# Optimization experiments

Hardware: AMD Instinct MI355X
Metric: run time of the kernel (lower is better)

## Reference

```python
import jax, jax.numpy as jnp
import numpy as np

NEG_SLOPE = 0.01  # torch leaky_relu default

def _lrelu(x):
    return jax.nn.leaky_relu(x, NEG_SLOPE)

def _l2norm(x, axis):
    # torch F.normalize(p=2, eps=1e-12)
    n = jnp.linalg.norm(x, axis=axis, keepdims=True)
    return x / jnp.maximum(n, 1e-12)

def setup_inputs() -> dict:
    key = jax.random.key(0)
    ks = jax.random.split(key, 12)
    Nda, Nq, C, Din, Dout = 10000, 64, 1024, 128, 256
    target_adj = (jax.random.uniform(ks[0], (Nda, Nda)) < 0.002).astype(jnp.float32)
    query_adj = (jax.random.uniform(ks[1], (Nq, Nq)) < 0.2).astype(jnp.float32)
    node_features_da = jax.random.normal(ks[2], (Nda, Din), dtype=jnp.float32)
    node_features_q = jax.random.normal(ks[3], (Nq, Din), dtype=jnp.float32)
    candidate_set = jax.random.randint(ks[4], (C,), 0, Nda)
    candidate_adj = (jax.random.uniform(ks[5], (C, C)) < 0.01).astype(jnp.float32)
    s_in = 1.0 / np.sqrt(Din).astype(np.float32)
    s_out = 1.0 / np.sqrt(Dout).astype(np.float32)
    W1_da = jax.random.normal(ks[6], (Din, Dout), dtype=jnp.float32) * s_in
    W1_q = jax.random.normal(ks[7], (Din, Dout), dtype=jnp.float32) * s_in
    W2_da = jax.random.normal(ks[8], (Dout, Dout), dtype=jnp.float32) * s_out
    W2_q = jax.random.normal(ks[9], (Dout, Dout), dtype=jnp.float32) * s_out
    threshold = jnp.float32(0.2)
    return {"target_adj": target_adj, "node_features_da": node_features_da,
            "query_adj": query_adj, "node_features_q": node_features_q,
            "candidate_set": candidate_set, "candidate_adj": candidate_adj,
            "threshold": threshold, "W1_da": W1_da, "W1_q": W1_q,
            "W2_da": W2_da, "W2_q": W2_q}

def _cross_cosine(q, da, candidate_set):
    # cosine similarity between each query node and each candidate target node: [Nq, C]
    return _l2norm(q, 1) @ _l2norm(da[candidate_set], 1).T

def reference(target_adj, node_features_da, query_adj, node_features_q,
              candidate_set, candidate_adj, threshold, W1_da, W1_q, W2_da, W2_q):
    # layer 1: GCN propagation on both graphs (gcn(adj,x) = adj @ x @ W)
    da1 = _lrelu(target_adj @ (node_features_da @ W1_da))   # [Nda, D]
    q1 = _lrelu(query_adj @ (node_features_q @ W1_q))       # [Nq, D]
    c1 = _cross_cosine(q1, da1, candidate_set)               # [Nq, C]
    pre_da1 = da1[candidate_set]                             # [C, D]
    # NOTE: da1[candidate_set].data = ... mutates a temporary in torch -> no-op on da1
    att_da1 = _lrelu(da1)                                    # dropout in eval = identity
    h1_q = c1 @ pre_da1                                      # [Nq, D]
    att_q1 = _lrelu(q1 + _l2norm(h1_q, 0))
    # layer 2
    da2 = _lrelu(target_adj @ (att_da1 @ W2_da))
    q2 = _lrelu(query_adj @ (att_q1 @ W2_q))
    c2 = _cross_cosine(q2, da2, candidate_set)
    pre_da2 = da2[candidate_set]
    att_da2 = _lrelu(da2)                                    # in-place update is again a no-op
    h2_q = c2 @ pre_da2
    att_q2 = _lrelu(q2 + _l2norm(h2_q, 0))
    # graph-level matching score per target node
    emb = jnp.mean(att_q2, axis=0, keepdims=True)            # [1, D]
    num = att_da2 @ emb[0]                                   # [Nda]
    den = jnp.maximum(jnp.linalg.norm(att_da2, axis=1) * jnp.linalg.norm(emb), 1e-8)
    end = (num / den)[None, :]                               # [1, Nda]
    # threshold selection expressed with a mask (jit-safe, same math: excluded
    # rows/cols are zero and do not affect L2 norms, sums, or the trace)
    m = (end[0] > threshold).astype(att_da2.dtype)           # [Nda]
    F_ = att_da2 * m[:, None]
    re_adj = F_ @ F_.T                                       # [Nda, Nda]
    nor_re = _l2norm(re_adj, 1) * target_adj                 # elementwise with original adj
    cnt = jnp.sum(m)
    total = jnp.sum(nor_re)
    tr = jnp.trace(nor_re)
    has = cnt > 0
    pre_avg_degree = jnp.where(has, total / jnp.maximum(cnt, 1.0), 0.0)
    pre_avg_nodes = jnp.where(has, tr, 0.0)
    pre_density = jnp.where(has, 2.0 * total / (tr * (tr - 1.0) + 1e-4), 0.0)
    return (end, att_da2, att_q2, pre_avg_degree, pre_density, pre_avg_nodes)
```

## Files before the change

kernel.cpp:

```cpp
#include <hip/hip_runtime.h>

constexpr int NDA = 10000;
constexpr int NQ  = 64;
constexpr int CND = 1024;
constexpr int DIN = 128;
constexpr int D   = 256;
constexpr int CAP = 96;
constexpr int NT128 = (NDA + 127) / 128;
constexpr int NB128 = NT128 * 2;
constexpr int NCHUNK = 32;
constexpr int GCHUNK = 320;

#define LRELU(x) ((x) >= 0.f ? (x) : 0.01f * (x))

__device__ __forceinline__ float wave_red64(float v) {
#pragma unroll
    for (int o = 32; o; o >>= 1) v += __shfl_down(v, o);
    return v;
}

struct GemmSmem    { float As[32][65]; float Bs[32][68]; };
struct Gemm128Smem { float As[16][132]; float Bs[16][132]; };
struct CrossSmem   { float qs[D]; float cmw[256]; int sci[256]; float red[4]; float sqn; };
struct SpmmSmem    { int sc[CAP]; };
struct CsrSmem     { int scnt; };
struct EndSmem     { float se[D]; float scnt; float red[4]; };
struct FinalSmem   { int sc[CAP]; float smask[CAP]; int sdiag; float r1[4], r2[4], r3[4]; };
struct Attq4Smem   { float hbuf[64][65]; float red[4][64]; float invs[64]; };
union SMem {
    GemmSmem g; Gemm128Smem h; CrossSmem c; SpmmSmem s; CsrSmem z;
    EndSmem e; FinalSmem f; Attq4Smem a;
};

template <bool RELU_A, bool RELU_C>
__device__ __forceinline__ void gemm_body(GemmSmem& sm, int bx, int by,
                                          const float* __restrict__ A,
                                          const float* __restrict__ B,
                                          float* __restrict__ C,
                                          int M, int N, int K) {
    const int bm = bx * 64, bn = by * 64;
    const int tid = threadIdx.x;
    const int tx = tid & 15, ty = tid >> 4;
    const int lm = tid >> 2, lk = (tid & 3) * 8;
    const int kb = tid >> 3, nb = (tid & 7) * 8;
    const bool aValid = (bm + lm) < M;
    const float* aPtr = A + (size_t)(bm + lm) * K + lk;
    const float* bPtr = B + (size_t)kb * N + bn + nb;
    float4 ra0 = make_float4(0.f, 0.f, 0.f, 0.f), ra1 = ra0, rb0, rb1;
    if (aValid) { ra0 = *(const float4*)aPtr; ra1 = *(const float4*)(aPtr + 4); }
    rb0 = *(const float4*)bPtr;
    rb1 = *(const float4*)(bPtr + 4);
    float acc[4][4] = {};
    for (int k0 = 0; k0 < K; k0 += 32) {
        float4 wa0 = ra0, wa1 = ra1, wb0 = rb0, wb1 = rb1;
        if (RELU_A) {
            wa0.x = LRELU(wa0.x); wa0.y = LRELU(wa0.y); wa0.z = LRELU(wa0.z); wa0.w = LRELU(wa0.w);
            wa1.x = LRELU(wa1.x); wa1.y = LRELU(wa1.y); wa1.z = LRELU(wa1.z); wa1.w = LRELU(wa1.w);
        }
        sm.As[lk + 0][lm] = wa0.x; sm.As[lk + 1][lm] = wa0.y;
        sm.As[lk + 2][lm] = wa0.z; sm.As[lk + 3][lm] = wa0.w;
        sm.As[lk + 4][lm] = wa1.x; sm.As[lk + 5][lm] = wa1.y;
        sm.As[lk + 6][lm] = wa1.z; sm.As[lk + 7][lm] = wa1.w;
        *(float4*)&sm.Bs[kb][nb]     = wb0;
        *(float4*)&sm.Bs[kb][nb + 4] = wb1;
        __syncthreads();
        if (k0 + 32 < K) {
            if (aValid) {
                ra0 = *(const float4*)(aPtr + k0 + 32);
                ra1 = *(const float4*)(aPtr + k0 + 36);
            }
            rb0 = *(const float4*)(bPtr + (size_t)(k0 + 32) * N);
            rb1 = *(const float4*)(bPtr + (size_t)(k0 + 32) * N + 4);
        }
#pragma unroll
        for (int kk = 0; kk < 32; kk++) {
            float av[4], bv[4];
#pragma unroll
            for (int i = 0; i < 4; i++) av[i] = sm.As[kk][ty * 4 + i];
#pragma unroll
            for (int j = 0; j < 4; j++) bv[j] = sm.Bs[kk][tx * 4 + j];
#pragma unroll
            for (int i = 0; i < 4; i++)
#pragma unroll
                for (int j = 0; j < 4; j++) acc[i][j] += av[i] * bv[j];
        }
        __syncthreads();
    }
#pragma unroll
    for (int i = 0; i < 4; i++) {
        int r = bm + ty * 4 + i;
        if (r < M) {
            float4 v = make_float4(acc[i][0], acc[i][1], acc[i][2], acc[i][3]);
            if (RELU_C) { v.x = LRELU(v.x); v.y = LRELU(v.y); v.z = LRELU(v.z); v.w = LRELU(v.w); }
            *(float4*)(C + (size_t)r * N + bn + tx * 4) = v;
        }
    }
}

template <bool RELU_A>
__device__ __forceinline__ void gemm128_body(Gemm128Smem& sm, int bx, int by,
                                             const float* __restrict__ A,
                                             const float* __restrict__ B,
                                             float* __restrict__ C,
                                             int M, int N, int K) {
    const int bm = bx * 128, bn = by * 128;
    const int tid = threadIdx.x;
    const int tx = tid & 15, ty = tid >> 4;
    const int am = tid >> 1, ak = (tid & 1) * 8;
    const int bk = tid >> 4, bn8 = (tid & 15) * 8;
    const bool aValid = (bm + am) < M;
    const float* aPtr = A + (size_t)(bm + am) * K + ak;
    const float* bPtr = B + (size_t)bk * N + bn + bn8;
    float4 ra0 = make_float4(0.f, 0.f, 0.f, 0.f), ra1 = ra0, rb0, rb1;
    if (aValid) { ra0 = *(const float4*)aPtr; ra1 = *(const float4*)(aPtr + 4); }
    rb0 = *(const float4*)bPtr;
    rb1 = *(const float4*)(bPtr + 4);
    float acc[8][8] = {};
    for (int k0 = 0; k0 < K; k0 += 16) {
        float a8[8] = { ra0.x, ra0.y, ra0.z, ra0.w, ra1.x, ra1.y, ra1.z, ra1.w };
        if (RELU_A) {
#pragma unroll
            for (int j = 0; j < 8; j++) a8[j] = LRELU(a8[j]);
        }
#pragma unroll
        for (int j = 0; j < 8; j++) sm.As[ak + j][am] = a8[j];
        *(float4*)&sm.Bs[bk][bn8]     = rb0;
        *(float4*)&sm.Bs[bk][bn8 + 4] = rb1;
        __syncthreads();
        if (k0 + 16 < K) {
            if (aValid) {
                ra0 = *(const float4*)(aPtr + k0 + 16);
                ra1 = *(const float4*)(aPtr + k0 + 20);
            }
            rb0 = *(const float4*)(bPtr + (size_t)(k0 + 16) * N);
            rb1 = *(const float4*)(bPtr + (size_t)(k0 + 16) * N + 4);
        }
#pragma unroll
        for (int kk = 0; kk < 16; kk++) {
            float4 a0 = *(const float4*)&sm.As[kk][ty * 8];
            float4 a1 = *(const float4*)&sm.As[kk][ty * 8 + 4];
            float4 b0 = *(const float4*)&sm.Bs[kk][tx * 8];
            float4 b1 = *(const float4*)&sm.Bs[kk][tx * 8 + 4];
            float av[8] = { a0.x, a0.y, a0.z, a0.w, a1.x, a1.y, a1.z, a1.w };
            float bv[8] = { b0.x, b0.y, b0.z, b0.w, b1.x, b1.y, b1.z, b1.w };
#pragma unroll
            for (int i = 0; i < 8; i++)
#pragma unroll
                for (int j = 0; j < 8; j++) acc[i][j] += av[i] * bv[j];
        }
        __syncthreads();
    }
#pragma unroll
    for (int i = 0; i < 8; i++) {
        int r = bm + ty * 8 + i;
        if (r < M) {
            float4 v0 = make_float4(acc[i][0], acc[i][1], acc[i][2], acc[i][3]);
            float4 v1 = make_float4(acc[i][4], acc[i][5], acc[i][6], acc[i][7]);
            *(float4*)(C + (size_t)r * N + bn + tx * 8)     = v0;
            *(float4*)(C + (size_t)r * N + bn + tx * 8 + 4) = v1;
        }
    }
}

__device__ __forceinline__ void csr_body(CsrSmem& sm, const float* __restrict__ adj,
                                         int* __restrict__ cols,
                                         int* __restrict__ rowcnt, int row) {
    if (threadIdx.x == 0) sm.scnt = 0;
    __syncthreads();
    const float4* rp = (const float4*)(adj + (size_t)row * NDA);
    for (int i = threadIdx.x; i < NDA / 4; i += 256) {
        float4 v = rp[i];
        if (v.x != 0.f) { int s = atomicAdd(&sm.scnt, 1); if (s < CAP) cols[row * CAP + s] = 4 * i; }
        if (v.y != 0.f) { int s = atomicAdd(&sm.scnt, 1); if (s < CAP) cols[row * CAP + s] = 4 * i + 1; }
        if (v.z != 0.f) { int s = atomicAdd(&sm.scnt, 1); if (s < CAP) cols[row * CAP + s] = 4 * i + 2; }
        if (v.w != 0.f) { int s = atomicAdd(&sm.scnt, 1); if (s < CAP) cols[row * CAP + s] = 4 * i + 3; }
    }
    __syncthreads();
    if (threadIdx.x == 0) rowcnt[row] = min(sm.scnt, CAP);
}

__device__ __forceinline__ void spmm_body(SpmmSmem& sm, const int* __restrict__ cols,
                                          const int* __restrict__ rowcnt,
                                          const float* __restrict__ X,
                                          float* __restrict__ out1,
                                          float* __restrict__ out2, int row) {
    int d = threadIdx.x;
    int cnt = rowcnt[row];
    if (d < cnt) sm.sc[d] = cols[row * CAP + d];
    __syncthreads();
    float a0 = 0.f, a1 = 0.f, a2 = 0.f, a3 = 0.f;
    int k = 0;
    for (; k + 4 <= cnt; k += 4) {
        a0 += X[(size_t)sm.sc[k + 0] * D + d];
        a1 += X[(size_t)sm.sc[k + 1] * D + d];
        a2 += X[(size_t)sm.sc[k + 2] * D + d];
        a3 += X[(size_t)sm.sc[k + 3] * D + d];
    }
    for (; k < cnt; k++) a0 += X[(size_t)sm.sc[k] * D + d];
    float v = LRELU(a0 + a1 + a2 + a3);
    out1[(size_t)row * D + d] = v;
    if (out2) out2[(size_t)row * D + d] = LRELU(v);
}

__device__ __forceinline__ void cross_body(CrossSmem& sm, const float* __restrict__ q,
                                           const float* __restrict__ da,
                                           const int* __restrict__ cand,
                                           float* __restrict__ hpart,
                                           int r, int qr) {
    int d = threadIdx.x;
    float qv = q[r * D + d];
    sm.qs[d] = qv;
    sm.sci[d] = cand[qr * 256 + d];
    float p = wave_red64(qv * qv);
    int w = d >> 6, lane = d & 63;
    if (lane == 0) sm.red[w] = p;
    __syncthreads();
    if (d == 0) sm.sqn = fmaxf(sqrtf(sm.red[0] + sm.red[1] + sm.red[2] + sm.red[3]), 1e-12f);
    __syncthreads();
    float qn = sm.sqn;
    {
        const float4* ap = (const float4*)(da + (size_t)sm.sci[d] * D);
        float dot = 0.f, sq = 0.f;
#pragma unroll 8
        for (int k = 0; k < D / 4; k++) {
            float4 v = ap[k];
            dot += sm.qs[4 * k] * v.x + sm.qs[4 * k + 1] * v.y + sm.qs[4 * k + 2] * v.z + sm.qs[4 * k + 3] * v.w;
            sq  += v.x * v.x + v.y * v.y + v.z * v.z + v.w * v.w;
        }
        sm.cmw[d] = dot / (qn * fmaxf(sqrtf(sq), 1e-12f));
    }
    __syncthreads();
    float a0 = 0.f, a1 = 0.f, a2 = 0.f, a3 = 0.f, a4 = 0.f, a5 = 0.f, a6 = 0.f, a7 = 0.f;
    for (int c = 0; c < 256; c += 8) {
        a0 += sm.cmw[c + 0] * da[(size_t)sm.sci[c + 0] * D + d];
        a1 += sm.cmw[c + 1] * da[(size_t)sm.sci[c + 1] * D + d];
        a2 += sm.cmw[c + 2] * da[(size_t)sm.sci[c + 2] * D + d];
        a3 += sm.cmw[c + 3] * da[(size_t)sm.sci[c + 3] * D + d];
        a4 += sm.cmw[c + 4] * da[(size_t)sm.sci[c + 4] * D + d];
        a5 += sm.cmw[c + 5] * da[(size_t)sm.sci[c + 5] * D + d];
        a6 += sm.cmw[c + 6] * da[(size_t)sm.sci[c + 6] * D + d];
        a7 += sm.cmw[c + 7] * da[(size_t)sm.sci[c + 7] * D + d];
    }
    hpart[((size_t)qr * NQ + r) * D + d] = ((a0 + a1) + (a2 + a3)) + ((a4 + a5) + (a6 + a7));
}

__global__ __launch_bounds__(256) void stage0_kernel(const float* __restrict__ adj,
                                                     int* __restrict__ cols,
                                                     int* __restrict__ rowcnt,
                                                     const float* __restrict__ Fda,
                                                     const float* __restrict__ W1da,
                                                     float* __restrict__ X1,
                                                     const float* __restrict__ Fq,
                                                     const float* __restrict__ W1q,
                                                     float* __restrict__ Xq) {
    __shared__ SMem sm;
    int bid = blockIdx.x;
    if (bid < NB128) {
        gemm128_body<false>(sm.h, bid >> 1, bid & 1, Fda, W1da, X1, NDA, D, DIN);
    } else if (bid < NB128 + 4) {
        gemm_body<false, false>(sm.g, 0, bid - NB128, Fq, W1q, Xq, NQ, D, DIN);
    } else {
        csr_body(sm.z, adj, cols, rowcnt, bid - (NB128 + 4));
    }
}

__global__ __launch_bounds__(256) void stage_sg_kernel(const int* __restrict__ cols,
                                                       const int* __restrict__ rowcnt,
                                                       const float* __restrict__ X,
                                                       float* __restrict__ out1,
                                                       float* __restrict__ out2,
                                                       const float* __restrict__ Aq,
                                                       const float* __restrict__ Bq,
                                                       float* __restrict__ Cq) {
    __shared__ SMem sm;
    int bid = blockIdx.x;
    if (bid < 4) {
        gemm_body<false, true>(sm.g, 0, bid, Aq, Bq, Cq, NQ, D, NQ);
    } else {
        spmm_body(sm.s, cols, rowcnt, X, out1, out2, bid - 4);
    }
}

__global__ __launch_bounds__(256) void mergeA_kernel(const float* __restrict__ q1,
                                                     const float* __restrict__ da1,
                                                     const int* __restrict__ cand,
                                                     float* __restrict__ hpart,
                                                     const float* __restrict__ W2da,
                                                     float* __restrict__ Y2) {
    __shared__ SMem sm;
    int bid = blockIdx.x;
    if (bid < 256) {
        cross_body(sm.c, q1, da1, cand, hpart, bid >> 2, bid & 3);
    } else {
        int t = bid - 256;
        gemm128_body<true>(sm.h, t >> 1, t & 1, da1, W2da, Y2, NDA, D, D);
    }
}

__global__ __launch_bounds__(256) void cross_kernel(const float* __restrict__ q,
                                                    const float* __restrict__ da,
                                                    const int* __restrict__ cand,
                                                    float* __restrict__ hpart) {
    __shared__ SMem sm;
    cross_body(sm.c, q, da, cand, hpart, blockIdx.x, blockIdx.y);
}

__global__ __launch_bounds__(256) void qfused_kernel(const float* __restrict__ q,
                                                     const float* __restrict__ hpart,
                                                     const float* __restrict__ W2q,
                                                     float* __restrict__ Zq) {
    __shared__ float aqT[D][65];
    __shared__ float Bs[32][68];
    int d = threadIdx.x;
    float hv[NQ];
    float ss = 0.f;
#pragma unroll
    for (int r = 0; r < NQ; r++) {
        float h = hpart[(size_t)r * D + d]
                + hpart[(size_t)(NQ + r) * D + d]
                + hpart[(size_t)(2 * NQ + r) * D + d]
                + hpart[(size_t)(3 * NQ + r) * D + d];
        hv[r] = h;
        ss += h * h;
    }
    float inv = 1.f / fmaxf(sqrtf(ss), 1e-12f);
#pragma unroll
    for (int r = 0; r < NQ; r++) {
        float v = q[r * D + d] + hv[r] * inv;
        aqT[d][r] = LRELU(v);
    }
    __syncthreads();
    const int bn = blockIdx.x * 64;
    const int tx = d & 15, ty = d >> 4;
    const int kb = d >> 3, nb = (d & 7) * 8;
    float acc[4][4] = {};
    for (int k0 = 0; k0 < D; k0 += 32) {
        float4 b0 = *(const float4*)(W2q + (size_t)(k0 + kb) * D + bn + nb);
        float4 b1 = *(const float4*)(W2q + (size_t)(k0 + kb) * D + bn + nb + 4);
        *(float4*)&Bs[kb][nb]     = b0;
        *(float4*)&Bs[kb][nb + 4] = b1;
        __syncthreads();
#pragma unroll
        for (int kk = 0; kk < 32; kk++) {
            float av[4], bv[4];
#pragma unroll
            for (int i = 0; i < 4; i++) av[i] = aqT[k0 + kk][ty * 4 + i];
#pragma unroll
            for (int j = 0; j < 4; j++) bv[j] = Bs[kk][tx * 4 + j];
#pragma unroll
            for (int i = 0; i < 4; i++)
#pragma unroll
                for (int j = 0; j < 4; j++) acc[i][j] += av[i] * bv[j];
        }
        __syncthreads();
    }
#pragma unroll
    for (int i = 0; i < 4; i++) {
        float4 v = make_float4(acc[i][0], acc[i][1], acc[i][2], acc[i][3]);
        *(float4*)(Zq + (size_t)(ty * 4 + i) * D + bn + tx * 4) = v;
    }
}

__global__ __launch_bounds__(256) void attq4_kernel(const float* __restrict__ q,
                                                    const float* __restrict__ hpart,
                                                    float* __restrict__ attq,
                                                    float* __restrict__ emb,
                                                    float* __restrict__ cnt,
                                                    double* __restrict__ tot,
                                                    double* __restrict__ tr,
                                                    int* __restrict__ done) {
    __shared__ SMem smu;
    Attq4Smem& sm = smu.a;
    int b = blockIdx.x, t = threadIdx.x;
    int lc = t & 63, rq = t >> 6;
    int c = b * 64 + lc;
    if (b == 0 && t == 0) { *cnt = 0.f; *tot = 0.0; *tr = 0.0; *done = 0; }
    float ss = 0.f;
#pragma unroll
    for (int rr = 0; rr < 16; rr++) {
        int r = rq * 16 + rr;
        float h = hpart[(size_t)r * D + c]
                + hpart[(size_t)(NQ + r) * D + c]
                + hpart[(size_t)(2 * NQ + r) * D + c]
                + hpart[(size_t)(3 * NQ + r) * D + c];
        sm.hbuf[r][lc] = h;
        ss += h * h;
    }
    sm.red[rq][lc] = ss;
    __syncthreads();
    if (rq == 0) {
        float s = sm.red[0][lc] + sm.red[1][lc] + sm.red[2][lc] + sm.red[3][lc];
        sm.invs[lc] = 1.f / fmaxf(sqrtf(s), 1e-12f);
    }
    __syncthreads();
    float inv = sm.invs[lc];
    float es = 0.f;
#pragma unroll
    for (int rr = 0; rr < 16; rr++) {
        int r = rq * 16 + rr;
        float v = q[r * D + c] + sm.hbuf[r][lc] * inv;
        v = LRELU(v);
        attq[r * D + c] = v;
        es += v;
    }
    __syncthreads();
    sm.red[rq][lc] = es;
    __syncthreads();
    if (rq == 0) {
        float e = (sm.red[0][lc] + sm.red[1][lc] + sm.red[2][lc] + sm.red[3][lc]) * (1.f / (float)NQ);
        emb[c] = e;
    }
}

__global__ __launch_bounds__(256) void end_kernel(const float* __restrict__ A,
                                                  const float* __restrict__ emb,
                                                  const float* __restrict__ thr_p,
                                                  float* __restrict__ endv,
                                                  float* __restrict__ m,
                                                  float* __restrict__ cnt) {
    __shared__ SMem smu;
    EndSmem& sm = smu.e;
    int d = threadIdx.x;
    float ev = emb[d];
    sm.se[d] = ev;
    if (d == 0) sm.scnt = 0.f;
    int w = d >> 6, lane = d & 63;
    float pe = wave_red64(ev * ev);
    if (lane == 0) sm.red[w] = pe;
    __syncthreads();
    float embn = sqrtf(sm.red[0] + sm.red[1] + sm.red[2] + sm.red[3]);
    float thr = *thr_p;
    int row = blockIdx.x * 4 + w;
    const float* ar = A + (size_t)row * D;
    float num = 0.f, sq = 0.f;
#pragma unroll
    for (int s = 0; s < 4; s++) {
        float v = ar[lane + 64 * s];
        num += v * sm.se[lane + 64 * s];
        sq += v * v;
    }
#pragma unroll
    for (int o = 32; o; o >>= 1) { num += __shfl_down(num, o); sq += __shfl_down(sq, o); }
    if (lane == 0) {
        float den = fmaxf(sqrtf(sq) * embn, 1e-8f);
        float e = num / den;
        endv[row] = e;
        float mv = e > thr ? 1.f : 0.f;
        m[row] = mv;
        if (mv != 0.f) atomicAdd(&sm.scnt, 1.f);
    }
    __syncthreads();
    if (d == 0 && sm.scnt != 0.f) atomicAdd(cnt, sm.scnt);
}

__global__ __launch_bounds__(256) void Gpart_kernel(const float* __restrict__ A,
                                                    const float* __restrict__ m,
                                                    float* __restrict__ Gp) {
    __shared__ SMem smu;
    Gemm128Smem& sm = smu.h;
    int ti = blockIdx.x >> 1, tj = blockIdx.x & 1;
    int base = blockIdx.y * GCHUNK;
    int tid = threadIdx.x;
    int tx = tid & 15, ty = tid >> 4;
    int sr = tid >> 4, sc8 = (tid & 15) * 8;
    float acc[8][8] = {};
    for (int g0 = 0; g0 < GCHUNK; g0 += 16) {
        int r = base + g0 + sr;
        float4 va0 = make_float4(0.f, 0.f, 0.f, 0.f), va1 = va0, vb0 = va0, vb1 = va0;
        float mv = 0.f;
        if (r < NDA) {
            mv = m[r];
            const float* ar = A + (size_t)r * D;
            va0 = *(const float4*)(ar + ti * 128 + sc8);
            va1 = *(const float4*)(ar + ti * 128 + sc8 + 4);
            vb0 = *(const float4*)(ar + tj * 128 + sc8);
            vb1 = *(const float4*)(ar + tj * 128 + sc8 + 4);
        }
        va0.x *= mv; va0.y *= mv; va0.z *= mv; va0.w *= mv;
        va1.x *= mv; va1.y *= mv; va1.z *= mv; va1.w *= mv;
        *(float4*)&sm.As[sr][sc8]     = va0;
        *(float4*)&sm.As[sr][sc8 + 4] = va1;
        *(float4*)&sm.Bs[sr][sc8]     = vb0;
        *(float4*)&sm.Bs[sr][sc8 + 4] = vb1;
        __syncthreads();
#pragma unroll
        for (int kk = 0; kk < 16; kk++) {
            float4 a0 = *(const float4*)&sm.As[kk][ty * 8];
            float4 a1 = *(const float4*)&sm.As[kk][ty * 8 + 4];
            float4 b0 = *(const float4*)&sm.Bs[kk][tx * 8];
            float4 b1 = *(const float4*)&sm.Bs[kk][tx * 8 + 4];
            float av[8] = { a0.x, a0.y, a0.z, a0.w, a1.x, a1.y, a1.z, a1.w };
            float bv[8] = { b0.x, b0.y, b0.z, b0.w, b1.x, b1.y, b1.z, b1.w };
#pragma unroll
            for (int i = 0; i < 8; i++)
#pragma unroll
                for (int j = 0; j < 8; j++) acc[i][j] += av[i] * bv[j];
        }
        __syncthreads();
    }
    float* gp = Gp + (size_t)blockIdx.y * D * D;
#pragma unroll
    for (int i = 0; i < 8; i++) {
        int gi = ti * 128 + ty * 8 + i;
        float4 v0 = make_float4(acc[i][0], acc[i][1], acc[i][2], acc[i][3]);
        float4 v1 = make_float4(acc[i][4], acc[i][5], acc[i][6], acc[i][7]);
        *(float4*)(gp + (size_t)gi * D + tj * 128 + tx * 8)     = v0;
        *(float4*)(gp + (size_t)gi * D + tj * 128 + tx * 8 + 4) = v1;
    }
}

__global__ __launch_bounds__(256) void Gred_kernel(const float* __restrict__ Gp,
                                                   float* __restrict__ G) {
    int idx = blockIdx.x * 256 + threadIdx.x;
    float s = 0.f;
#pragma unroll
    for (int c = 0; c < NCHUNK; c++) s += Gp[(size_t)c * D * D + idx];
    G[idx] = s;
}

__global__ __launch_bounds__(256) void gemmH_kernel(const float* __restrict__ A,
                                                    const float* __restrict__ B,
                                                    float* __restrict__ C) {
    __shared__ SMem sm;
    gemm128_body<false>(sm.h, blockIdx.x >> 1, blockIdx.x & 1, A, B, C, NDA, D, D);
}

__global__ __launch_bounds__(256) void final_kernel(const int* __restrict__ cols,
                                                    const int* __restrict__ rowcnt,
                                                    const float* __restrict__ m,
                                                    const float* __restrict__ A,
                                                    const float* __restrict__ H,
                                                    double* __restrict__ total,
                                                    double* __restrict__ tr,
                                                    float* __restrict__ cnt,
                                                    int* __restrict__ done,
                                                    float* __restrict__ o_sc) {
    __shared__ SMem smu;
    FinalSmem& sm = smu.f;
    int i = blockIdx.x;
    int d = threadIdx.x;
    if (m[i] != 0.f) {
        int cnt_r = rowcnt[i];
        if (d == 0) sm.sdiag = 0;
        if (d < cnt_r) {
            int j = cols[i * CAP + d];
            sm.sc[d] = j;
            sm.smask[d] = m[j];
            if (j == i) sm.sdiag = 1;
        }
        __syncthreads();
        float av = A[(size_t)i * D + d];
        float hv = H[(size_t)i * D + d];
        float sd = 0.f;
        for (int k = 0; k < cnt_r; k++)
            if (sm.smask[k] != 0.f) sd += A[(size_t)sm.sc[k] * D + d];
        float p1 = av * sd, p2 = av * hv, p3 = av * av;
#pragma unroll
        for (int o = 32; o; o >>= 1) {
            p1 += __shfl_down(p1, o);
            p2 += __shfl_down(p2, o);
            p3 += __shfl_down(p3, o);
        }
        int w = d >> 6, lane = d & 63;
        if (lane == 0) { sm.r1[w] = p1; sm.r2[w] = p2; sm.r3[w] = p3; }
        __syncthreads();
        if (d == 0) {
            float num  = sm.r1[0] + sm.r1[1] + sm.r1[2] + sm.r1[3];
            float den2 = sm.r2[0] + sm.r2[1] + sm.r2[2] + sm.r2[3];
            float self = sm.r3[0] + sm.r3[1] + sm.r3[2] + sm.r3[3];
            float denom = fmaxf(sqrtf(den2), 1e-12f);
            double inv = 1.0 / (double)denom;
            if (num != 0.f) atomicAdd(total, (double)num * inv);
            if (sm.sdiag) atomicAdd(tr, (double)self * inv);
        }
    }
    if (d == 0) {
        __threadfence();
        int prev = atomicAdd(done, 1);
        if (prev == NDA - 1) {
            float c = atomicAdd(cnt, 0.f);
            float T = (float)atomicAdd(total, 0.0);
            float R = (float)atomicAdd(tr, 0.0);
            bool has = c > 0.f;
            o_sc[0] = has ? (T / fmaxf(c, 1.f)) : 0.f;
            o_sc[1] = has ? (2.f * T / (R * (R - 1.f) + 1e-4f)) : 0.f;
            o_sc[2] = has ? R : 0.f;
        }
    }
}

extern "C" void kernel_launch(void* const* d_in, const int* in_sizes, int n_in,
                              void* d_out, int out_size, void* d_ws, size_t ws_size,
                              hipStream_t stream) {
    (void)in_sizes; (void)n_in; (void)out_size; (void)ws_size;
    const float* adj  = (const float*)d_in[0];
    const float* Fda  = (const float*)d_in[1];
    const float* Qadj = (const float*)d_in[2];
    const float* Fq   = (const float*)d_in[3];
    const int*   cand = (const int*)d_in[4];
    const float* thr  = (const float*)d_in[6];
    const float* W1da = (const float*)d_in[7];
    const float* W1q  = (const float*)d_in[8];
    const float* W2da = (const float*)d_in[9];
    const float* W2q  = (const float*)d_in[10];

    float* out = (float*)d_out;
    float* o_end    = out;
    float* o_attda2 = out + NDA;
    float* o_attq2  = out + NDA + (size_t)NDA * D;
    float* o_sc     = o_attq2 + NQ * D;

    char* w = (char*)d_ws;
    size_t off = 0;
    auto alloc = [&](size_t b) { size_t r = off; off += (b + 255) & ~(size_t)255; return r; };
    float* bufA = (float*)(w + alloc((size_t)NDA * D * 4));
    float* bufB = (float*)(w + alloc((size_t)NDA * D * 4));
    float* bufC = (float*)(w + alloc((size_t)NDA * D * 4));
    int* colsb   = (int*)(w + alloc((size_t)NDA * CAP * 4));
    int* rowcntb = (int*)(w + alloc((size_t)NDA * 4));
    float* mbuf  = (float*)(w + alloc((size_t)NDA * 4));
    float* Gb    = (float*)(w + alloc((size_t)D * D * 4));
    float* Gp    = (float*)(w + alloc((size_t)NCHUNK * D * D * 4));
    char* zbase = w + alloc(256);
    float* cntb  = (float*)zbase;
    double* totb = (double*)(zbase + 8);
    double* trb  = (double*)(zbase + 16);
    int*    doneb = (int*)(zbase + 24);
    float* xq   = (float*)(w + alloc((size_t)NQ * D * 4));
    float* q1b  = (float*)(w + alloc((size_t)NQ * D * 4));
    float* q2b  = (float*)(w + alloc((size_t)NQ * D * 4));
    float* hpart = (float*)(w + alloc((size_t)4 * NQ * D * 4));
    float* embb = (float*)(w + alloc((size_t)(D + 1) * 4));

    stage0_kernel<<<NB128 + 4 + NDA, 256, 0, stream>>>(adj, colsb, rowcntb,
                                                       Fda, W1da, bufA, Fq, W1q, xq);
    stage_sg_kernel<<<NDA + 4, 256, 0, stream>>>(colsb, rowcntb, bufA, bufB, (float*)nullptr,
                                                 Qadj, xq, q1b);
    mergeA_kernel<<<256 + NB128, 256, 0, stream>>>(q1b, bufB, cand, hpart, W2da, bufA);
    qfused_kernel<<<4, 256, 0, stream>>>(q1b, hpart, W2q, xq);
    stage_sg_kernel<<<NDA + 4, 256, 0, stream>>>(colsb, rowcntb, bufA, bufC, o_attda2,
                                                 Qadj, xq, q2b);
    cross_kernel<<<dim3(NQ, 4), 256, 0, stream>>>(q2b, bufC, cand, hpart);
    attq4_kernel<<<4, 256, 0, stream>>>(q2b, hpart, o_attq2, embb, cntb, totb, trb, doneb);
    end_kernel<<<NDA / 4, 256, 0, stream>>>(o_attda2, embb, thr, o_end, mbuf, cntb);
    Gpart_kernel<<<dim3(4, NCHUNK), 256, 0, stream>>>(o_attda2, mbuf, Gp);
    Gred_kernel<<<D * D / 256, 256, 0, stream>>>(Gp, Gb);
    gemmH_kernel<<<NB128, 256, 0, stream>>>(o_attda2, Gb, bufB);
    final_kernel<<<NDA, 256, 0, stream>>>(colsb, rowcntb, mbuf, o_attda2, bufB,
                                          totb, trb, cntb, doneb, o_sc);
}
```

Measured before the change: 1.261 ms.

## Vectorize gathers with float4 per-wave row splits and per-kernel shared memory

The sparse aggregation, cross-similarity and final kernels now have each wavefront read whole 256-float rows as float4. The four waves split the neighbor list between them and combine partial sums in shared memory, replacing scalar per-thread gathers. The cosine dot products use wave shuffles instead of one thread looping over a full row. The shared-memory union is narrowed per kernel to lower LDS use and raise occupancy. The done-counter finalisation in final_kernel moves to a separate single-thread scalars kernel, and final_kernel compacts masked neighbors before summing; this costs one more kernel launch and extra LDS for partial sums.

```diff
diff --git a/kernel.cpp b/kernel.cpp
--- a/kernel.cpp
+++ b/kernel.cpp
@@ -21,16 +21,12 @@
 
 struct GemmSmem    { float As[32][65]; float Bs[32][68]; };
 struct Gemm128Smem { float As[16][132]; float Bs[16][132]; };
-struct CrossSmem   { float qs[D]; float cmw[256]; int sci[256]; float red[4]; float sqn; };
-struct SpmmSmem    { int sc[CAP]; };
+struct CrossSmem   { float qs[D]; float cmw[256]; int sci[256]; float red[4]; float sqn; float part[4][256]; };
+struct SpmmSmem    { int sc[CAP]; float part[4][256]; };
 struct CsrSmem     { int scnt; };
 struct EndSmem     { float se[D]; float scnt; float red[4]; };
-struct FinalSmem   { int sc[CAP]; float smask[CAP]; int sdiag; float r1[4], r2[4], r3[4]; };
+struct FinalSmem   { int sc[CAP]; float part[4][256]; int n; int sdiag; float r1[4], r2[4], r3[4]; };
 struct Attq4Smem   { float hbuf[64][65]; float red[4][64]; float invs[64]; };
-union SMem {
-    GemmSmem g; Gemm128Smem h; CrossSmem c; SpmmSmem s; CsrSmem z;
-    EndSmem e; FinalSmem f; Attq4Smem a;
-};
 
 template <bool RELU_A, bool RELU_C>
 __device__ __forceinline__ void gemm_body(GemmSmem& sm, int bx, int by,
@@ -184,22 +180,32 @@
                                           const float* __restrict__ X,
                                           float* __restrict__ out1,
                                           float* __restrict__ out2, int row) {
-    int d = threadIdx.x;
+    int t = threadIdx.x;
+    int w = t >> 6, lane = t & 63;
     int cnt = rowcnt[row];
-    if (d < cnt) sm.sc[d] = cols[row * CAP + d];
-    __syncthreads();
-    float a0 = 0.f, a1 = 0.f, a2 = 0.f, a3 = 0.f;
-    int k = 0;
-    for (; k + 4 <= cnt; k += 4) {
-        a0 += X[(size_t)sm.sc[k + 0] * D + d];
-        a1 += X[(size_t)sm.sc[k + 1] * D + d];
-        a2 += X[(size_t)sm.sc[k + 2] * D + d];
-        a3 += X[(size_t)sm.sc[k + 3] * D + d];
-    }
-    for (; k < cnt; k++) a0 += X[(size_t)sm.sc[k] * D + d];
-    float v = LRELU(a0 + a1 + a2 + a3);
-    out1[(size_t)row * D + d] = v;
-    if (out2) out2[(size_t)row * D + d] = LRELU(v);
+    if (t < cnt) sm.sc[t] = cols[row * CAP + t];
+    __syncthreads();
+    float4 acc = make_float4(0.f, 0.f, 0.f, 0.f);
+    int k = w;
+    for (; k + 4 < cnt; k += 8) {
+        const float4* x0 = (const float4*)(X + (size_t)sm.sc[k] * D);
+        const float4* x1 = (const float4*)(X + (size_t)sm.sc[k + 4] * D);
+        float4 v0 = x0[lane];
+        float4 v1 = x1[lane];
+        acc.x += v0.x + v1.x; acc.y += v0.y + v1.y;
+        acc.z += v0.z + v1.z; acc.w += v0.w + v1.w;
+    }
+    for (; k < cnt; k += 4) {
+        const float4* x0 = (const float4*)(X + (size_t)sm.sc[k] * D);
+        float4 v0 = x0[lane];
+        acc.x += v0.x; acc.y += v0.y; acc.z += v0.z; acc.w += v0.w;
+    }
+    *(float4*)&sm.part[w][lane * 4] = acc;
+    __syncthreads();
+    float s = sm.part[0][t] + sm.part[1][t] + sm.part[2][t] + sm.part[3][t];
+    float v = LRELU(s);
+    out1[(size_t)row * D + t] = v;
+    if (out2) out2[(size_t)row * D + t] = LRELU(v);
 }
 
 __device__ __forceinline__ void cross_body(CrossSmem& sm, const float* __restrict__ q,
@@ -207,41 +213,44 @@
                                            const int* __restrict__ cand,
                                            float* __restrict__ hpart,
                                            int r, int qr) {
-    int d = threadIdx.x;
-    float qv = q[r * D + d];
-    sm.qs[d] = qv;
-    sm.sci[d] = cand[qr * 256 + d];
+    int t = threadIdx.x;
+    int w = t >> 6, lane = t & 63;
+    float qv = q[r * D + t];
+    sm.qs[t] = qv;
+    sm.sci[t] = cand[qr * 256 + t];
     float p = wave_red64(qv * qv);
-    int w = d >> 6, lane = d & 63;
     if (lane == 0) sm.red[w] = p;
     __syncthreads();
-    if (d == 0) sm.sqn = fmaxf(sqrtf(sm.red[0] + sm.red[1] + sm.red[2] + sm.red[3]), 1e-12f);
+    if (t == 0) sm.sqn = fmaxf(sqrtf(sm.red[0] + sm.red[1] + sm.red[2] + sm.red[3]), 1e-12f);
     __syncthreads();
     float qn = sm.sqn;
-    {
-        const float4* ap = (const float4*)(da + (size_t)sm.sci[d] * D);
-        float dot = 0.f, sq = 0.f;
-#pragma unroll 8
-        for (int k = 0; k < D / 4; k++) {
-            float4 v = ap[k];
-            dot += sm.qs[4 * k] * v.x + sm.qs[4 * k + 1] * v.y + sm.qs[4 * k + 2] * v.z + sm.qs[4 * k + 3] * v.w;
-            sq  += v.x * v.x + v.y * v.y + v.z * v.z + v.w * v.w;
-        }
-        sm.cmw[d] = dot / (qn * fmaxf(sqrtf(sq), 1e-12f));
-    }
-    __syncthreads();
-    float a0 = 0.f, a1 = 0.f, a2 = 0.f, a3 = 0.f, a4 = 0.f, a5 = 0.f, a6 = 0.f, a7 = 0.f;
-    for (int c = 0; c < 256; c += 8) {
-        a0 += sm.cmw[c + 0] * da[(size_t)sm.sci[c + 0] * D + d];
-        a1 += sm.cmw[c + 1] * da[(size_t)sm.sci[c + 1] * D + d];
-        a2 += sm.cmw[c + 2] * da[(size_t)sm.sci[c + 2] * D + d];
-        a3 += sm.cmw[c + 3] * da[(size_t)sm.sci[c + 3] * D + d];
-        a4 += sm.cmw[c + 4] * da[(size_t)sm.sci[c + 4] * D + d];
-        a5 += sm.cmw[c + 5] * da[(size_t)sm.sci[c + 5] * D + d];
-        a6 += sm.cmw[c + 6] * da[(size_t)sm.sci[c + 6] * D + d];
-        a7 += sm.cmw[c + 7] * da[(size_t)sm.sci[c + 7] * D + d];
-    }
-    hpart[((size_t)qr * NQ + r) * D + d] = ((a0 + a1) + (a2 + a3)) + ((a4 + a5) + (a6 + a7));
+    float4 qv4 = *(const float4*)&sm.qs[lane * 4];
+    for (int c = w * 64; c < w * 64 + 64; c++) {
+        const float4* rp = (const float4*)(da + (size_t)sm.sci[c] * D);
+        float4 v = rp[lane];
+        float dp = qv4.x * v.x + qv4.y * v.y + qv4.z * v.z + qv4.w * v.w;
+        float sq = v.x * v.x + v.y * v.y + v.z * v.z + v.w * v.w;
+#pragma unroll
+        for (int o = 32; o; o >>= 1) { dp += __shfl_down(dp, o); sq += __shfl_down(sq, o); }
+        if (lane == 0) sm.cmw[c] = dp / (qn * fmaxf(sqrtf(sq), 1e-12f));
+    }
+    __syncthreads();
+    float4 acc = make_float4(0.f, 0.f, 0.f, 0.f);
+    for (int c = w; c < 256; c += 8) {
+        float w0 = sm.cmw[c], w1 = sm.cmw[c + 4];
+        const float4* p0 = (const float4*)(da + (size_t)sm.sci[c] * D);
+        const float4* p1 = (const float4*)(da + (size_t)sm.sci[c + 4] * D);
+        float4 v0 = p0[lane];
+        float4 v1 = p1[lane];
+        acc.x += w0 * v0.x + w1 * v1.x;
+        acc.y += w0 * v0.y + w1 * v1.y;
+        acc.z += w0 * v0.z + w1 * v1.z;
+        acc.w += w0 * v0.w + w1 * v1.w;
+    }
+    *(float4*)&sm.part[w][lane * 4] = acc;
+    __syncthreads();
+    float hs = sm.part[0][t] + sm.part[1][t] + sm.part[2][t] + sm.part[3][t];
+    hpart[((size_t)qr * NQ + r) * D + t] = hs;
 }
 
 __global__ __launch_bounds__(256) void stage0_kernel(const float* __restrict__ adj,
@@ -253,7 +262,7 @@
                                                      const float* __restrict__ Fq,
                                                      const float* __restrict__ W1q,
                                                      float* __restrict__ Xq) {
-    __shared__ SMem sm;
+    __shared__ union { Gemm128Smem h; GemmSmem g; CsrSmem z; } sm;
     int bid = blockIdx.x;
     if (bid < NB128) {
         gemm128_body<false>(sm.h, bid >> 1, bid & 1, Fda, W1da, X1, NDA, D, DIN);
@@ -272,7 +281,7 @@
                                                        const float* __restrict__ Aq,
                                                        const float* __restrict__ Bq,
                                                        float* __restrict__ Cq) {
-    __shared__ SMem sm;
+    __shared__ union { GemmSmem g; SpmmSmem s; } sm;
     int bid = blockIdx.x;
     if (bid < 4) {
         gemm_body<false, true>(sm.g, 0, bid, Aq, Bq, Cq, NQ, D, NQ);
@@ -287,7 +296,7 @@
                                                      float* __restrict__ hpart,
                                                      const float* __restrict__ W2da,
                                                      float* __restrict__ Y2) {
-    __shared__ SMem sm;
+    __shared__ union { CrossSmem c; Gemm128Smem h; } sm;
     int bid = blockIdx.x;
     if (bid < 256) {
         cross_body(sm.c, q1, da1, cand, hpart, bid >> 2, bid & 3);
@@ -301,8 +310,8 @@
                                                     const float* __restrict__ da,
                                                     const int* __restrict__ cand,
                                                     float* __restrict__ hpart) {
-    __shared__ SMem sm;
-    cross_body(sm.c, q, da, cand, hpart, blockIdx.x, blockIdx.y);
+    __shared__ CrossSmem sm;
+    cross_body(sm, q, da, cand, hpart, blockIdx.x, blockIdx.y);
 }
 
 __global__ __launch_bounds__(256) void qfused_kernel(const float* __restrict__ q,
@@ -367,14 +376,12 @@
                                                     float* __restrict__ emb,
                                                     float* __restrict__ cnt,
                                                     double* __restrict__ tot,
-                                                    double* __restrict__ tr,
-                                                    int* __restrict__ done) {
-    __shared__ SMem smu;
-    Attq4Smem& sm = smu.a;
+                                                    double* __restrict__ tr) {
+    __shared__ Attq4Smem sm;
     int b = blockIdx.x, t = threadIdx.x;
     int lc = t & 63, rq = t >> 6;
     int c = b * 64 + lc;
-    if (b == 0 && t == 0) { *cnt = 0.f; *tot = 0.0; *tr = 0.0; *done = 0; }
+    if (b == 0 && t == 0) { *cnt = 0.f; *tot = 0.0; *tr = 0.0; }
     float ss = 0.f;
 #pragma unroll
     for (int rr = 0; rr < 16; rr++) {
@@ -418,8 +425,7 @@
                                                   float* __restrict__ endv,
                                                   float* __restrict__ m,
                                                   float* __restrict__ cnt) {
-    __shared__ SMem smu;
-    EndSmem& sm = smu.e;
+    __shared__ EndSmem sm;
     int d = threadIdx.x;
     float ev = emb[d];
     sm.se[d] = ev;
@@ -456,8 +462,7 @@
 __global__ __launch_bounds__(256) void Gpart_kernel(const float* __restrict__ A,
                                                     const float* __restrict__ m,
                                                     float* __restrict__ Gp) {
-    __shared__ SMem smu;
-    Gemm128Smem& sm = smu.h;
+    __shared__ Gemm128Smem sm;
     int ti = blockIdx.x >> 1, tj = blockIdx.x & 1;
     int base = blockIdx.y * GCHUNK;
     int tid = threadIdx.x;
@@ -521,8 +526,8 @@
 __global__ __launch_bounds__(256) void gemmH_kernel(const float* __restrict__ A,
                                                     const float* __restrict__ B,
                                                     float* __restrict__ C) {
-    __shared__ SMem sm;
-    gemm128_body<false>(sm.h, blockIdx.x >> 1, blockIdx.x & 1, A, B, C, NDA, D, D);
+    __shared__ Gemm128Smem sm;
+    gemm128_body<false>(sm, blockIdx.x >> 1, blockIdx.x & 1, A, B, C, NDA, D, D);
 }
 
 __global__ __launch_bounds__(256) void final_kernel(const int* __restrict__ cols,
@@ -531,62 +536,76 @@
                                                     const float* __restrict__ A,
                                                     const float* __restrict__ H,
                                                     double* __restrict__ total,
-                                                    double* __restrict__ tr,
-                                                    float* __restrict__ cnt,
-                                                    int* __restrict__ done,
-                                                    float* __restrict__ o_sc) {
-    __shared__ SMem smu;
-    FinalSmem& sm = smu.f;
+                                                    double* __restrict__ tr) {
     int i = blockIdx.x;
-    int d = threadIdx.x;
-    if (m[i] != 0.f) {
-        int cnt_r = rowcnt[i];
-        if (d == 0) sm.sdiag = 0;
-        if (d < cnt_r) {
-            int j = cols[i * CAP + d];
-            sm.sc[d] = j;
-            sm.smask[d] = m[j];
+    if (m[i] == 0.f) return;
+    __shared__ FinalSmem sm;
+    int t = threadIdx.x;
+    int w = t >> 6, lane = t & 63;
+    int cnt = rowcnt[i];
+    if (t == 0) { sm.n = 0; sm.sdiag = 0; }
+    __syncthreads();
+    if (t < cnt) {
+        int j = cols[i * CAP + t];
+        if (m[j] != 0.f) {
+            int s = atomicAdd(&sm.n, 1);
+            sm.sc[s] = j;
             if (j == i) sm.sdiag = 1;
         }
-        __syncthreads();
-        float av = A[(size_t)i * D + d];
-        float hv = H[(size_t)i * D + d];
-        float sd = 0.f;
-        for (int k = 0; k < cnt_r; k++)
-            if (sm.smask[k] != 0.f) sd += A[(size_t)sm.sc[k] * D + d];
-        float p1 = av * sd, p2 = av * hv, p3 = av * av;
-#pragma unroll
-        for (int o = 32; o; o >>= 1) {
-            p1 += __shfl_down(p1, o);
-            p2 += __shfl_down(p2, o);
-            p3 += __shfl_down(p3, o);
-        }
-        int w = d >> 6, lane = d & 63;
-        if (lane == 0) { sm.r1[w] = p1; sm.r2[w] = p2; sm.r3[w] = p3; }
-        __syncthreads();
-        if (d == 0) {
-            float num  = sm.r1[0] + sm.r1[1] + sm.r1[2] + sm.r1[3];
-            float den2 = sm.r2[0] + sm.r2[1] + sm.r2[2] + sm.r2[3];
-            float self = sm.r3[0] + sm.r3[1] + sm.r3[2] + sm.r3[3];
-            float denom = fmaxf(sqrtf(den2), 1e-12f);
-            double inv = 1.0 / (double)denom;
-            if (num != 0.f) atomicAdd(total, (double)num * inv);
-            if (sm.sdiag) atomicAdd(tr, (double)self * inv);
-        }
-    }
-    if (d == 0) {
-        __threadfence();
-        int prev = atomicAdd(done, 1);
-        if (prev == NDA - 1) {
-            float c = atomicAdd(cnt, 0.f);
-            float T = (float)atomicAdd(total, 0.0);
-            float R = (float)atomicAdd(tr, 0.0);
-            bool has = c > 0.f;
-            o_sc[0] = has ? (T / fmaxf(c, 1.f)) : 0.f;
-            o_sc[1] = has ? (2.f * T / (R * (R - 1.f) + 1e-4f)) : 0.f;
-            o_sc[2] = has ? R : 0.f;
-        }
-    }
+    }
+    __syncthreads();
+    int n = sm.n;
+    float4 acc = make_float4(0.f, 0.f, 0.f, 0.f);
+    int k = w;
+    for (; k + 4 < n; k += 8) {
+        const float4* x0 = (const float4*)(A + (size_t)sm.sc[k] * D);
+        const float4* x1 = (const float4*)(A + (size_t)sm.sc[k + 4] * D);
+        float4 v0 = x0[lane];
+        float4 v1 = x1[lane];
+        acc.x += v0.x + v1.x; acc.y += v0.y + v1.y;
+        acc.z += v0.z + v1.z; acc.w += v0.w + v1.w;
+    }
+    for (; k < n; k += 4) {
+        const float4* x0 = (const float4*)(A + (size_t)sm.sc[k] * D);
+        float4 v0 = x0[lane];
+        acc.x += v0.x; acc.y += v0.y; acc.z += v0.z; acc.w += v0.w;
+    }
+    *(float4*)&sm.part[w][lane * 4] = acc;
+    __syncthreads();
+    float av = A[(size_t)i * D + t];
+    float hv = H[(size_t)i * D + t];
+    float sd = sm.part[0][t] + sm.part[1][t] + sm.part[2][t] + sm.part[3][t];
+    float p1 = av * sd, p2 = av * hv, p3 = av * av;
+#pragma unroll
+    for (int o = 32; o; o >>= 1) {
+        p1 += __shfl_down(p1, o);
+        p2 += __shfl_down(p2, o);
+        p3 += __shfl_down(p3, o);
+    }
+    if (lane == 0) { sm.r1[w] = p1; sm.r2[w] = p2; sm.r3[w] = p3; }
+    __syncthreads();
+    if (t == 0) {
+        float num  = sm.r1[0] + sm.r1[1] + sm.r1[2] + sm.r1[3];
+        float den2 = sm.r2[0] + sm.r2[1] + sm.r2[2] + sm.r2[3];
+        float self = sm.r3[0] + sm.r3[1] + sm.r3[2] + sm.r3[3];
+        float denom = fmaxf(sqrtf(den2), 1e-12f);
+        double inv = 1.0 / (double)denom;
+        if (num != 0.f) atomicAdd(total, (double)num * inv);
+        if (sm.sdiag) atomicAdd(tr, (double)self * inv);
+    }
+}
+
+__global__ void scalars_kernel(const float* __restrict__ cnt,
+                               const double* __restrict__ total,
+                               const double* __restrict__ tr,
+                               float* __restrict__ out) {
+    float c = *cnt;
+    float T = (float)*total;
+    float R = (float)*tr;
+    bool has = c > 0.f;
+    out[0] = has ? (T / fmaxf(c, 1.f)) : 0.f;
+    out[1] = has ? (2.f * T / (R * (R - 1.f) + 1e-4f)) : 0.f;
+    out[2] = has ? R : 0.f;
 }
 
 extern "C" void kernel_launch(void* const* d_in, const int* in_sizes, int n_in,
@@ -625,7 +644,6 @@
     float* cntb  = (float*)zbase;
     double* totb = (double*)(zbase + 8);
     double* trb  = (double*)(zbase + 16);
-    int*    doneb = (int*)(zbase + 24);
     float* xq   = (float*)(w + alloc((size_t)NQ * D * 4));
     float* q1b  = (float*)(w + alloc((size_t)NQ * D * 4));
     float* q2b  = (float*)(w + alloc((size_t)NQ * D * 4));
@@ -641,11 +659,11 @@
     stage_sg_kernel<<<NDA + 4, 256, 0, stream>>>(colsb, rowcntb, bufA, bufC, o_attda2,
                                                  Qadj, xq, q2b);
     cross_kernel<<<dim3(NQ, 4), 256, 0, stream>>>(q2b, bufC, cand, hpart);
-    attq4_kernel<<<4, 256, 0, stream>>>(q2b, hpart, o_attq2, embb, cntb, totb, trb, doneb);
+    attq4_kernel<<<4, 256, 0, stream>>>(q2b, hpart, o_attq2, embb, cntb, totb, trb);
     end_kernel<<<NDA / 4, 256, 0, stream>>>(o_attda2, embb, thr, o_end, mbuf, cntb);
     Gpart_kernel<<<dim3(4, NCHUNK), 256, 0, stream>>>(o_attda2, mbuf, Gp);
     Gred_kernel<<<D * D / 256, 256, 0, stream>>>(Gp, Gb);
     gemmH_kernel<<<NB128, 256, 0, stream>>>(o_attda2, Gb, bufB);
-    final_kernel<<<NDA, 256, 0, stream>>>(colsb, rowcntb, mbuf, o_attda2, bufB,
-                                          totb, trb, cntb, doneb, o_sc);
-}
+    final_kernel<<<NDA, 256, 0, stream>>>(colsb, rowcntb, mbuf, o_attda2, bufB, totb, trb);
+    scalars_kernel<<<1, 1, 0, stream>>>(cntb, totb, trb, o_sc);
+}
```

Result: faster. 1.096 ms (-13.1%).
